# Kernel optimization log

Hardware: AMD Instinct MI355X
Metric: run time of the kernel (lower is better)

The kernel has to match this reference:

```python
import jax, jax.numpy as jnp
import numpy as np

ALPHA = 0.1
EPS = 1e-12  # torch nf.normalize eps


def l2norm(x):
    # F.normalize(x, p=2, dim=-1)
    return x / jnp.maximum(jnp.linalg.norm(x, axis=-1, keepdims=True), EPS)


def setup_inputs() -> dict:
    key = jax.random.key(0)
    ks = jax.random.split(key, 8)
    N, E, F, H1, H2, C = 50000, 600000, 128, 256, 128, 40
    return {
        "x": jax.random.normal(ks[0], (N, F), jnp.float32),
        "neighbor_x": jax.random.normal(ks[1], (E, F), jnp.float32),
        "W1": jax.random.normal(ks[2], (F, H1), jnp.float32) / np.sqrt(F).astype(np.float32),
        "b1": jnp.zeros((H1,), jnp.float32),
        "W2": jax.random.normal(ks[3], (H1, H2), jnp.float32) / np.sqrt(H1).astype(np.float32),
        "b2": jnp.zeros((H2,), jnp.float32),
        "Wc": jax.random.normal(ks[4], (H2, C), jnp.float32) / np.sqrt(H2).astype(np.float32),
        "bc": jnp.zeros((C,), jnp.float32),
        "segment_ids": jax.random.randint(ks[5], (600000,), 0, 50000, dtype=jnp.int32),
    }


def reference(x, neighbor_x, W1, b1, W2, b2, Wc, bc, segment_ids):
    n_nodes = x.shape[0]
    seg_sum = lambda e: jax.ops.segment_sum(e, segment_ids, num_segments=n_nodes)

    # normalize node + neighbor features
    x = l2norm(x)                      # [N, F]
    nb = l2norm(neighbor_x)            # [E, F]

    # tran1 on nodes and neighbors
    h = x @ W1 + b1                    # [N, H1]
    n_h = nb @ W1 + b1                 # [E, H1]

    # app1: x <- (1-a) * (h + sum_neighbors(n_h)) + a * h
    x1 = (1.0 - ALPHA) * (h + seg_sum(n_h)) + ALPHA * h
    # acvt (ReLU; dropout p=0 -> identity) on x and neighbor embeddings
    x1 = jax.nn.relu(x1)
    n_r = jax.nn.relu(n_h)
    # app2: x <- (1-a) * (x + sum_neighbors(relu(n_h))) + a * h
    x2 = (1.0 - ALPHA) * (x1 + seg_sum(n_r)) + ALPHA * h

    # tran2 on nodes and (original tran1'd) neighbors
    h2 = x2 @ W2 + b2                  # [N, H2]
    n_h2 = n_h @ W2 + b2               # [E, H2]

    # app1 again
    x3 = (1.0 - ALPHA) * (h2 + seg_sum(n_h2)) + ALPHA * h2
    x3 = jax.nn.relu(x3)
    n_r2 = jax.nn.relu(n_h2)
    # app2 again
    x4 = (1.0 - ALPHA) * (x3 + seg_sum(n_r2)) + ALPHA * h2

    return x4 @ Wc + bc                # [N, C]
```

## Files before the change

kernel.cpp:

```cpp
#include <hip/hip_runtime.h>

constexpr int F  = 128;
constexpr int H1 = 256;
constexpr int H2 = 128;
constexpr int C  = 40;

using f32x4 = __attribute__((ext_vector_type(4))) float;
using f16x8 = __attribute__((ext_vector_type(8))) _Float16;
using f16x2 = __attribute__((ext_vector_type(2))) _Float16;

__device__ __forceinline__ float wave_sum64(float v) {
#pragma unroll
    for (int off = 32; off > 0; off >>= 1) v += __shfl_xor(v, off, 64);
    return v;
}

__global__ __launch_bounds__(256) void prep_weights(
    const float* __restrict__ W1, const float* __restrict__ W2,
    const float* __restrict__ Wc,
    _Float16* __restrict__ W1t, _Float16* __restrict__ W2t,
    _Float16* __restrict__ Wct)
{
    const int i = blockIdx.x * 256 + threadIdx.x;
    if (i < H1 * F) {
        const int j = i >> 7, f = i & 127;
        W1t[i] = (_Float16)W1[(size_t)f * H1 + j];
    }
    if (i < H2 * H1) {
        const int j = i >> 8, k = i & 255;
        W2t[i] = (_Float16)W2[(size_t)k * H2 + j];
    }
    if (i < 48 * F) {
        const int c = i >> 7, k = i & 127;
        Wct[i] = (c < C) ? (_Float16)Wc[(size_t)k * C + c] : (_Float16)0.f;
    }
}

__global__ __launch_bounds__(256) void k_hist(
    const int* __restrict__ seg, int* __restrict__ hist, int E)
{
    const int e = blockIdx.x * 256 + threadIdx.x;
    if (e < E) atomicAdd(&hist[seg[e]], 1);
}

__global__ __launch_bounds__(256) void k_scan1(
    const int* __restrict__ hist, int* __restrict__ bsum, int N)
{
    __shared__ int s[256];
    const int t = threadIdx.x;
    const int i = blockIdx.x * 256 + t;
    s[t] = (i < N) ? hist[i] : 0;
    __syncthreads();
#pragma unroll
    for (int off = 128; off > 0; off >>= 1) {
        if (t < off) s[t] += s[t + off];
        __syncthreads();
    }
    if (t == 0) bsum[blockIdx.x] = s[0];
}

__global__ __launch_bounds__(256) void k_scan2(int* __restrict__ bsum, int B)
{
    __shared__ int s[256];
    const int t = threadIdx.x;
    const int v = (t < B) ? bsum[t] : 0;
    s[t] = v;
    __syncthreads();
#pragma unroll
    for (int off = 1; off < 256; off <<= 1) {
        const int u = (t >= off) ? s[t - off] : 0;
        __syncthreads();
        s[t] += u;
        __syncthreads();
    }
    if (t < B) bsum[t] = s[t] - v;
}

__global__ __launch_bounds__(256) void k_scan3(
    const int* __restrict__ hist, const int* __restrict__ bsum,
    int* __restrict__ start, int* __restrict__ cursor, int N, int E)
{
    __shared__ int s[256];
    const int t = threadIdx.x;
    const int i = blockIdx.x * 256 + t;
    const int v = (i < N) ? hist[i] : 0;
    s[t] = v;
    __syncthreads();
#pragma unroll
    for (int off = 1; off < 256; off <<= 1) {
        const int u = (t >= off) ? s[t - off] : 0;
        __syncthreads();
        s[t] += u;
        __syncthreads();
    }
    if (i < N) {
        start[i]  = bsum[blockIdx.x] + s[t] - v;
        cursor[i] = 0;
    }
    if (i == 0) start[N] = E;
}

__global__ __launch_bounds__(256) void k_scatter(
    const int* __restrict__ seg, const int* __restrict__ start,
    int* __restrict__ cursor, int* __restrict__ ord, int E)
{
    const int e = blockIdx.x * 256 + threadIdx.x;
    if (e < E) {
        const int s = seg[e];
        const int r = atomicAdd(&cursor[s], 1);
        ord[start[s] + r] = e;
    }
}

__global__ __launch_bounds__(256, 3) void edge_kernel8(
    const float* __restrict__ nbx, const int* __restrict__ seg,
    const int* __restrict__ ord, const int* __restrict__ start,
    const _Float16* __restrict__ W1t, const float* __restrict__ b1,
    const _Float16* __restrict__ W2t, const float* __restrict__ b2,
    float* __restrict__ Sx, float* __restrict__ S2, float* __restrict__ S4,
    int E)
{
    __shared__ _Float16 s_h[64][264];

    const int tid   = threadIdx.x;
    const int lane  = tid & 63;
    const int w     = tid >> 6;
    const int wrow0 = w * 16;
    const int wbase = blockIdx.x * 64 + wrow0;
    const int mrow  = lane & 15;
    const int kgrp  = lane >> 4;

    const int  p    = wbase + mrow;
    const bool pin  = (p < E);
    const int  edge = pin ? ord[p] : 0;

    float va[16][2];
#pragma unroll
    for (int r = 0; r < 16; ++r) {
        const int er = __shfl(edge, r);
        const bool v = (wbase + r < E);
        va[r][0] = v ? nbx[(size_t)er * F + lane] : 0.f;
        va[r][1] = v ? nbx[(size_t)er * F + 64 + lane] : 0.f;
    }

    const int sv = pin ? seg[edge] : -1;
    int fl = 0;
    if (pin) {
        const int s0 = start[sv], s1 = start[sv + 1];
        fl = (s0 >= wbase) && (s1 <= wbase + 16);
    }

#pragma unroll
    for (int r = 0; r < 16; ++r) {
        const float ss = wave_sum64(va[r][0] * va[r][0] + va[r][1] * va[r][1]);
        const float sc = 1.0f / fmaxf(sqrtf(ss), 1e-12f);
        va[r][0] *= sc; va[r][1] *= sc;
        s_h[wrow0 + r][lane]      = (_Float16)va[r][0];
        s_h[wrow0 + r][64 + lane] = (_Float16)va[r][1];
    }

    {
        float a0 = 0.f, a1v = 0.f;
        int cur = __shfl(sv, 0);
        int cf  = __shfl(fl, 0);
#pragma unroll
        for (int r = 0; r < 16; ++r) {
            a0 += va[r][0]; a1v += va[r][1];
            const int nxt = (r < 15) ? __shfl(sv, r + 1) : -2;
            if (nxt != cur) {
                if (cur >= 0) {
                    float* d = &Sx[(size_t)cur * F + lane];
                    if (cf) { d[0] = a0; d[64] = a1v; }
                    else    { atomicAdd(d, a0); atomicAdd(d + 64, a1v); }
                }
                a0 = 0.f; a1v = 0.f; cur = nxt;
                if (r < 15) cf = __shfl(fl, r + 1);
            }
        }
    }

    __syncthreads();

    f16x8 aA[4][4];
#pragma unroll
    for (int m = 0; m < 4; ++m)
#pragma unroll
        for (int kk = 0; kk < 4; ++kk)
            aA[m][kk] = *(const f16x8*)&s_h[m * 16 + mrow][kk * 32 + kgrp * 8];

    asm volatile("s_waitcnt lgkmcnt(0)" ::: "memory");
    __builtin_amdgcn_sched_barrier(0);
    __syncthreads();

    {
        const int colbase = w * 64 + mrow;
        float bj1[4];
#pragma unroll
        for (int ct = 0; ct < 4; ++ct) bj1[ct] = b1[colbase + ct * 16];

        f16x8 b[4], bn[4];
#pragma unroll
        for (int kk = 0; kk < 4; ++kk)
            b[kk] = *(const f16x8*)&W1t[(size_t)colbase * F + kk * 32 + kgrp * 8];

#pragma unroll
        for (int ct = 0; ct < 4; ++ct) {
            const int col = colbase + ct * 16;
            if (ct < 3) {
#pragma unroll
                for (int kk = 0; kk < 4; ++kk)
                    bn[kk] = *(const f16x8*)&W1t[(size_t)(col + 16) * F + kk * 32 + kgrp * 8];
            }
            f32x4 acc[4];
#pragma unroll
            for (int m = 0; m < 4; ++m) acc[m] = (f32x4){0.f, 0.f, 0.f, 0.f};
#pragma unroll
            for (int kk = 0; kk < 4; ++kk)
#pragma unroll
                for (int m = 0; m < 4; ++m)
                    acc[m] = __builtin_amdgcn_mfma_f32_16x16x32_f16(aA[m][kk], b[kk], acc[m], 0, 0, 0);
#pragma unroll
            for (int m = 0; m < 4; ++m)
#pragma unroll
                for (int q = 0; q < 4; ++q)
                    s_h[m * 16 + kgrp * 4 + q][col] = (_Float16)(acc[m][q] + bj1[ct]);
#pragma unroll
            for (int kk = 0; kk < 4; ++kk) b[kk] = bn[kk];
        }
    }
    __syncthreads();

#pragma unroll
    for (int half = 0; half < 2; ++half) {
        const int c0 = half * 128 + 2 * lane;
        float a0 = 0.f, a1v = 0.f;
        int cur = __shfl(sv, 0);
        int cf  = __shfl(fl, 0);
#pragma unroll
        for (int r = 0; r < 16; ++r) {
            const f16x2 pv = *(const f16x2*)&s_h[wrow0 + r][c0];
            a0  += fmaxf((float)pv[0], 0.f);
            a1v += fmaxf((float)pv[1], 0.f);
            const int nxt = (r < 15) ? __shfl(sv, r + 1) : -2;
            if (nxt != cur) {
                if (cur >= 0) {
                    float* d = &S2[(size_t)cur * H1 + c0];
                    if (cf) { *(float2*)d = make_float2(a0, a1v); }
                    else    { atomicAdd(d, a0); atomicAdd(d + 1, a1v); }
                }
                a0 = 0.f; a1v = 0.f; cur = nxt;
                if (r < 15) cf = __shfl(fl, r + 1);
            }
        }
    }

    f32x4 acc2[2][4];
#pragma unroll
    for (int ct = 0; ct < 2; ++ct)
#pragma unroll
        for (int m = 0; m < 4; ++m) acc2[ct][m] = (f32x4){0.f, 0.f, 0.f, 0.f};

    float bj2[2];
#pragma unroll
    for (int ct = 0; ct < 2; ++ct) bj2[ct] = b2[w * 32 + ct * 16 + mrow];

#pragma unroll
    for (int ct = 0; ct < 2; ++ct) {
        const int col = w * 32 + ct * 16 + mrow;
        f16x8 b[8];
#pragma unroll
        for (int k0 = 0; k0 < 8; ++k0)
            b[k0] = *(const f16x8*)&W2t[(size_t)col * H1 + k0 * 32 + kgrp * 8];
#pragma unroll
        for (int m = 0; m < 4; ++m) {
            f16x8 a[8];
#pragma unroll
            for (int k0 = 0; k0 < 8; ++k0)
                a[k0] = *(const f16x8*)&s_h[m * 16 + mrow][k0 * 32 + kgrp * 8];
#pragma unroll
            for (int k0 = 0; k0 < 8; ++k0)
                acc2[ct][m] = __builtin_amdgcn_mfma_f32_16x16x32_f16(a[k0], b[k0], acc2[ct][m], 0, 0, 0);
        }
    }
    __syncthreads();

#pragma unroll
    for (int ct = 0; ct < 2; ++ct) {
        const int col = w * 32 + ct * 16 + mrow;
#pragma unroll
        for (int m = 0; m < 4; ++m)
#pragma unroll
            for (int q = 0; q < 4; ++q)
                s_h[m * 16 + kgrp * 4 + q][col] = (_Float16)(acc2[ct][m][q] + bj2[ct]);
    }
    __syncthreads();

    {
        const int c0 = 2 * lane;
        float a0 = 0.f, a1v = 0.f;
        int cur = __shfl(sv, 0);
        int cf  = __shfl(fl, 0);
#pragma unroll
        for (int r = 0; r < 16; ++r) {
            const f16x2 pv = *(const f16x2*)&s_h[wrow0 + r][c0];
            a0  += fmaxf((float)pv[0], 0.f);
            a1v += fmaxf((float)pv[1], 0.f);
            const int nxt = (r < 15) ? __shfl(sv, r + 1) : -2;
            if (nxt != cur) {
                if (cur >= 0) {
                    float* d = &S4[(size_t)cur * H2 + c0];
                    if (cf) { *(float2*)d = make_float2(a0, a1v); }
                    else    { atomicAdd(d, a0); atomicAdd(d + 1, a1v); }
                }
                a0 = 0.f; a1v = 0.f; cur = nxt;
                if (r < 15) cf = __shfl(fl, r + 1);
            }
        }
    }
}

__global__ __launch_bounds__(256, 2) void node_kernel7(
    const float* __restrict__ x,
    const _Float16* __restrict__ W1t, const float* __restrict__ b1,
    const _Float16* __restrict__ W2t, const float* __restrict__ b2,
    const _Float16* __restrict__ Wct, const float* __restrict__ bc,
    const float* __restrict__ Sx, const float* __restrict__ S2,
    const float* __restrict__ S4, const int* __restrict__ start,
    float* __restrict__ out, int N)
{
    __shared__ _Float16 s_a[4][32][264];

    const int tid  = threadIdx.x;
    const int lane = tid & 63;
    const int w    = tid >> 6;
    const int n0   = blockIdx.x * 64 + w * 16;
    const int mrow = lane & 15;
    const int kgrp = lane >> 4;

#pragma unroll
    for (int r = 0; r < 16; ++r) {
        const int n = n0 + r;
        float v0 = 0.f, v1 = 0.f, u0 = 0.f, u1 = 0.f;
        if (n < N) {
            v0 = x[(size_t)n * F + lane];
            v1 = x[(size_t)n * F + 64 + lane];
            u0 = Sx[(size_t)n * F + lane];
            u1 = Sx[(size_t)n * F + 64 + lane];
        }
        const float ss = wave_sum64(v0 * v0 + v1 * v1);
        const float sc = 1.0f / fmaxf(sqrtf(ss), 1e-12f);
        s_a[w][r][lane]           = (_Float16)(v0 * sc);
        s_a[w][r][64 + lane]      = (_Float16)(v1 * sc);
        s_a[w][16 + r][lane]      = (_Float16)u0;
        s_a[w][16 + r][64 + lane] = (_Float16)u1;
    }

    float cntq[4];
#pragma unroll
    for (int q = 0; q < 4; ++q) {
        const int n = n0 + kgrp * 4 + q;
        cntq[q] = (n < N) ? (float)(start[n + 1] - start[n]) : 0.f;
    }

    asm volatile("s_waitcnt lgkmcnt(0)" ::: "memory");
    __builtin_amdgcn_sched_barrier(0);

    f16x8 aA[2][4];
#pragma unroll
    for (int m = 0; m < 2; ++m)
#pragma unroll
        for (int kk = 0; kk < 4; ++kk)
            aA[m][kk] = *(const f16x8*)&s_a[w][m * 16 + mrow][kk * 32 + kgrp * 8];

#pragma unroll
    for (int n = 0; n < 16; ++n) {
        const int col = n * 16 + mrow;
        f32x4 accH = {0.f, 0.f, 0.f, 0.f};
        f32x4 accS = {0.f, 0.f, 0.f, 0.f};
#pragma unroll
        for (int kk = 0; kk < 4; ++kk) {
            const f16x8 b = *(const f16x8*)&W1t[(size_t)col * F + kk * 32 + kgrp * 8];
            accH = __builtin_amdgcn_mfma_f32_16x16x32_f16(aA[0][kk], b, accH, 0, 0, 0);
            accS = __builtin_amdgcn_mfma_f32_16x16x32_f16(aA[1][kk], b, accS, 0, 0, 0);
        }
        const float bj = b1[col];
#pragma unroll
        for (int q = 0; q < 4; ++q) {
            const int row = kgrp * 4 + q;
            const int n_  = n0 + row;
            const float h  = accH[q] + bj;
            const float S1 = accS[q] + cntq[q] * bj;
            const float x1 = fmaxf(h + 0.9f * S1, 0.f);
            const float s2v = (n_ < N) ? S2[(size_t)n_ * H1 + col] : 0.f;
            const float x2 = 0.9f * (x1 + s2v) + 0.1f * h;
            s_a[w][row][col]      = (_Float16)x2;
            s_a[w][16 + row][col] = (_Float16)S1;
        }
    }

    asm volatile("s_waitcnt lgkmcnt(0)" ::: "memory");
    __builtin_amdgcn_sched_barrier(0);

    f16x8 aB[2][8];
#pragma unroll
    for (int m = 0; m < 2; ++m)
#pragma unroll
        for (int k0 = 0; k0 < 8; ++k0)
            aB[m][k0] = *(const f16x8*)&s_a[w][m * 16 + mrow][k0 * 32 + kgrp * 8];

#pragma unroll
    for (int n = 0; n < 8; ++n) {
        const int col = n * 16 + mrow;
        f32x4 accH = {0.f, 0.f, 0.f, 0.f};
        f32x4 accS = {0.f, 0.f, 0.f, 0.f};
#pragma unroll
        for (int k0 = 0; k0 < 8; ++k0) {
            const f16x8 b = *(const f16x8*)&W2t[(size_t)col * H1 + k0 * 32 + kgrp * 8];
            accH = __builtin_amdgcn_mfma_f32_16x16x32_f16(aB[0][k0], b, accH, 0, 0, 0);
            accS = __builtin_amdgcn_mfma_f32_16x16x32_f16(aB[1][k0], b, accS, 0, 0, 0);
        }
        const float bj = b2[col];
#pragma unroll
        for (int q = 0; q < 4; ++q) {
            const int row = kgrp * 4 + q;
            const int n_  = n0 + row;
            const float h2 = accH[q] + bj;
            const float S3 = accS[q] + cntq[q] * bj;
            const float x3 = fmaxf(h2 + 0.9f * S3, 0.f);
            const float s4v = (n_ < N) ? S4[(size_t)n_ * H2 + col] : 0.f;
            s_a[w][row][col] = (_Float16)(0.9f * (x3 + s4v) + 0.1f * h2);
        }
    }

    asm volatile("s_waitcnt lgkmcnt(0)" ::: "memory");
    __builtin_amdgcn_sched_barrier(0);

    f16x8 aC[4];
#pragma unroll
    for (int kk = 0; kk < 4; ++kk)
        aC[kk] = *(const f16x8*)&s_a[w][mrow][kk * 32 + kgrp * 8];

#pragma unroll
    for (int n = 0; n < 3; ++n) {
        const int col = n * 16 + mrow;
        f32x4 acc = {0.f, 0.f, 0.f, 0.f};
#pragma unroll
        for (int kk = 0; kk < 4; ++kk) {
            const f16x8 b = *(const f16x8*)&Wct[(size_t)col * F + kk * 32 + kgrp * 8];
            acc = __builtin_amdgcn_mfma_f32_16x16x32_f16(aC[kk], b, acc, 0, 0, 0);
        }
        if (col < C) {
            const float bcc = bc[col];
#pragma unroll
            for (int q = 0; q < 4; ++q) {
                const int n_ = n0 + kgrp * 4 + q;
                if (n_ < N) out[(size_t)n_ * C + col] = acc[q] + bcc;
            }
        }
    }
}

extern "C" void kernel_launch(void* const* d_in, const int* in_sizes, int n_in,
                              void* d_out, int out_size, void* d_ws, size_t ws_size,
                              hipStream_t stream) {
    const float* x   = (const float*)d_in[0];
    const float* nbx = (const float*)d_in[1];
    const float* W1  = (const float*)d_in[2];
    const float* b1  = (const float*)d_in[3];
    const float* W2  = (const float*)d_in[4];
    const float* b2  = (const float*)d_in[5];
    const float* Wc  = (const float*)d_in[6];
    const float* bc  = (const float*)d_in[7];
    const int*   seg = (const int*)d_in[8];

    const int N = in_sizes[0] / F;
    const int E = in_sizes[8];
    float* out = (float*)d_out;

    float* Sx    = (float*)d_ws;
    float* S2    = Sx + (size_t)N * F;
    float* S4    = S2 + (size_t)N * H1;
    int*   hist  = (int*)(S4 + (size_t)N * H2);
    int*   cursor= hist + N;
    int*   bsum  = cursor + N;
    int*   start = bsum + 256;
    int*   ord   = start + (N + 1);
    char*  wrest = (char*)(ord + E);
    _Float16* W1t = (_Float16*)(((uintptr_t)wrest + 15) & ~(uintptr_t)15);
    _Float16* W2t = W1t + (size_t)H1 * F;
    _Float16* Wct = W2t + (size_t)H2 * H1;

    const size_t zero_bytes = ((size_t)N * (F + H1 + H2)) * 4 + (size_t)N * 8 + 1024;
    hipMemsetAsync(d_ws, 0, zero_bytes, stream);

    prep_weights<<<128, 256, 0, stream>>>(W1, W2, Wc, W1t, W2t, Wct);

    const int B = (N + 255) / 256;
    k_hist   <<<(E + 255) / 256, 256, 0, stream>>>(seg, hist, E);
    k_scan1  <<<B, 256, 0, stream>>>(hist, bsum, N);
    k_scan2  <<<1, 256, 0, stream>>>(bsum, B);
    k_scan3  <<<B, 256, 0, stream>>>(hist, bsum, start, cursor, N, E);
    k_scatter<<<(E + 255) / 256, 256, 0, stream>>>(seg, start, cursor, ord, E);

    edge_kernel8<<<(E + 63) / 64, 256, 0, stream>>>(
        nbx, seg, ord, start, W1t, b1, W2t, b2, Sx, S2, S4, E);
    node_kernel7<<<(N + 63) / 64, 256, 0, stream>>>(
        x, W1t, b1, W2t, b2, Wct, bc, Sx, S2, S4, start, out, N);
}
```

Before: 565.7 us.

## Process two 64-edge tiles per block with upfront gathers and split LDS buffers

The edge kernel now handles 128 edges per block as two 64-edge tiles. All neighbor-row gathers for both tiles are issued at the start, so the second tile's global loads overlap the first tile's normalization, matmuls and scatter. The single shared buffer becomes two (normalized inputs and layer-1 output), MFMA sections are wrapped in raised wave priority, and A fragments are now read from LDS inside the loop rather than held in registers. This doubles the register footprint for gathered rows, which may hurt occupancy under the 3-block launch bound, and adds more block barriers.

```diff
diff --git a/kernel.cpp b/kernel.cpp
--- a/kernel.cpp
+++ b/kernel.cpp
@@ -112,7 +112,7 @@
     }
 }
 
-__global__ __launch_bounds__(256, 3) void edge_kernel8(
+__global__ __launch_bounds__(256, 3) void edge_kernel9(
     const float* __restrict__ nbx, const int* __restrict__ seg,
     const int* __restrict__ ord, const int* __restrict__ start,
     const _Float16* __restrict__ W1t, const float* __restrict__ b1,
@@ -120,202 +120,196 @@
     float* __restrict__ Sx, float* __restrict__ S2, float* __restrict__ S4,
     int E)
 {
-    __shared__ _Float16 s_h[64][264];
+    __shared__ _Float16 s_nb[64][136];
+    __shared__ _Float16 s_nh[64][264];
 
     const int tid   = threadIdx.x;
     const int lane  = tid & 63;
     const int w     = tid >> 6;
     const int wrow0 = w * 16;
-    const int wbase = blockIdx.x * 64 + wrow0;
     const int mrow  = lane & 15;
     const int kgrp  = lane >> 4;
-
-    const int  p    = wbase + mrow;
-    const bool pin  = (p < E);
-    const int  edge = pin ? ord[p] : 0;
-
-    float va[16][2];
-#pragma unroll
-    for (int r = 0; r < 16; ++r) {
-        const int er = __shfl(edge, r);
-        const bool v = (wbase + r < E);
-        va[r][0] = v ? nbx[(size_t)er * F + lane] : 0.f;
-        va[r][1] = v ? nbx[(size_t)er * F + 64 + lane] : 0.f;
-    }
-
-    const int sv = pin ? seg[edge] : -1;
-    int fl = 0;
-    if (pin) {
-        const int s0 = start[sv], s1 = start[sv + 1];
-        fl = (s0 >= wbase) && (s1 <= wbase + 16);
-    }
-
-#pragma unroll
-    for (int r = 0; r < 16; ++r) {
-        const float ss = wave_sum64(va[r][0] * va[r][0] + va[r][1] * va[r][1]);
-        const float sc = 1.0f / fmaxf(sqrtf(ss), 1e-12f);
-        va[r][0] *= sc; va[r][1] *= sc;
-        s_h[wrow0 + r][lane]      = (_Float16)va[r][0];
-        s_h[wrow0 + r][64 + lane] = (_Float16)va[r][1];
-    }
-
-    {
-        float a0 = 0.f, a1v = 0.f;
-        int cur = __shfl(sv, 0);
-        int cf  = __shfl(fl, 0);
+    const int base  = blockIdx.x * 128;
+
+    int edg[2], sv[2], fl[2];
+    float va[2][16][2];
+#pragma unroll
+    for (int t = 0; t < 2; ++t) {
+        const int wbase = base + t * 64 + wrow0;
+        const int p     = wbase + mrow;
+        const bool pin  = (p < E);
+        edg[t] = pin ? ord[p] : 0;
+        sv[t]  = pin ? seg[edg[t]] : -1;
+        fl[t]  = 0;
+        if (pin) {
+            const int s0 = start[sv[t]], s1 = start[sv[t] + 1];
+            fl[t] = (s0 >= wbase) && (s1 <= wbase + 16);
+        }
 #pragma unroll
         for (int r = 0; r < 16; ++r) {
-            a0 += va[r][0]; a1v += va[r][1];
-            const int nxt = (r < 15) ? __shfl(sv, r + 1) : -2;
-            if (nxt != cur) {
-                if (cur >= 0) {
-                    float* d = &Sx[(size_t)cur * F + lane];
-                    if (cf) { d[0] = a0; d[64] = a1v; }
-                    else    { atomicAdd(d, a0); atomicAdd(d + 64, a1v); }
+            const int er = __shfl(edg[t], r);
+            const bool v = (wbase + r < E);
+            va[t][r][0] = v ? nbx[(size_t)er * F + lane] : 0.f;
+            va[t][r][1] = v ? nbx[(size_t)er * F + 64 + lane] : 0.f;
+        }
+    }
+
+#pragma unroll
+    for (int t = 0; t < 2; ++t) {
+#pragma unroll
+        for (int r = 0; r < 16; ++r) {
+            const float ss = wave_sum64(va[t][r][0] * va[t][r][0] +
+                                        va[t][r][1] * va[t][r][1]);
+            const float sc = 1.0f / fmaxf(sqrtf(ss), 1e-12f);
+            va[t][r][0] *= sc; va[t][r][1] *= sc;
+            s_nb[wrow0 + r][lane]      = (_Float16)va[t][r][0];
+            s_nb[wrow0 + r][64 + lane] = (_Float16)va[t][r][1];
+        }
+
+        {
+            float a0 = 0.f, a1v = 0.f;
+            int cur = __shfl(sv[t], 0);
+            int cf  = __shfl(fl[t], 0);
+#pragma unroll
+            for (int r = 0; r < 16; ++r) {
+                a0 += va[t][r][0]; a1v += va[t][r][1];
+                const int nxt = (r < 15) ? __shfl(sv[t], r + 1) : -2;
+                if (nxt != cur) {
+                    if (cur >= 0) {
+                        float* d = &Sx[(size_t)cur * F + lane];
+                        if (cf) { d[0] = a0; d[64] = a1v; }
+                        else    { atomicAdd(d, a0); atomicAdd(d + 64, a1v); }
+                    }
+                    a0 = 0.f; a1v = 0.f; cur = nxt;
+                    if (r < 15) cf = __shfl(fl[t], r + 1);
                 }
-                a0 = 0.f; a1v = 0.f; cur = nxt;
-                if (r < 15) cf = __shfl(fl, r + 1);
             }
         }
-    }
-
-    __syncthreads();
-
-    f16x8 aA[4][4];
-#pragma unroll
-    for (int m = 0; m < 4; ++m)
-#pragma unroll
-        for (int kk = 0; kk < 4; ++kk)
-            aA[m][kk] = *(const f16x8*)&s_h[m * 16 + mrow][kk * 32 + kgrp * 8];
-
-    asm volatile("s_waitcnt lgkmcnt(0)" ::: "memory");
-    __builtin_amdgcn_sched_barrier(0);
-    __syncthreads();
-
-    {
-        const int colbase = w * 64 + mrow;
-        float bj1[4];
-#pragma unroll
-        for (int ct = 0; ct < 4; ++ct) bj1[ct] = b1[colbase + ct * 16];
-
-        f16x8 b[4], bn[4];
-#pragma unroll
-        for (int kk = 0; kk < 4; ++kk)
-            b[kk] = *(const f16x8*)&W1t[(size_t)colbase * F + kk * 32 + kgrp * 8];
-
-#pragma unroll
-        for (int ct = 0; ct < 4; ++ct) {
-            const int col = colbase + ct * 16;
-            if (ct < 3) {
-#pragma unroll
-                for (int kk = 0; kk < 4; ++kk)
-                    bn[kk] = *(const f16x8*)&W1t[(size_t)(col + 16) * F + kk * 32 + kgrp * 8];
+        __syncthreads();
+
+        {
+            const int colbase = w * 64 + mrow;
+            float bj1[4];
+#pragma unroll
+            for (int ct = 0; ct < 4; ++ct) bj1[ct] = b1[colbase + ct * 16];
+
+            f16x8 b[4], bn[4];
+#pragma unroll
+            for (int kk = 0; kk < 4; ++kk)
+                b[kk] = *(const f16x8*)&W1t[(size_t)colbase * F + kk * 32 + kgrp * 8];
+
+#pragma unroll
+            for (int ct = 0; ct < 4; ++ct) {
+                const int col = colbase + ct * 16;
+                if (ct < 3) {
+#pragma unroll
+                    for (int kk = 0; kk < 4; ++kk)
+                        bn[kk] = *(const f16x8*)&W1t[(size_t)(col + 16) * F + kk * 32 + kgrp * 8];
+                }
+                f32x4 acc[4];
+#pragma unroll
+                for (int m = 0; m < 4; ++m) acc[m] = (f32x4){0.f, 0.f, 0.f, 0.f};
+                __builtin_amdgcn_s_setprio(1);
+#pragma unroll
+                for (int m = 0; m < 4; ++m) {
+                    f16x8 a[4];
+#pragma unroll
+                    for (int kk = 0; kk < 4; ++kk)
+                        a[kk] = *(const f16x8*)&s_nb[m * 16 + mrow][kk * 32 + kgrp * 8];
+#pragma unroll
+                    for (int kk = 0; kk < 4; ++kk)
+                        acc[m] = __builtin_amdgcn_mfma_f32_16x16x32_f16(a[kk], b[kk], acc[m], 0, 0, 0);
+                }
+                __builtin_amdgcn_s_setprio(0);
+#pragma unroll
+                for (int m = 0; m < 4; ++m)
+#pragma unroll
+                    for (int q = 0; q < 4; ++q)
+                        s_nh[m * 16 + kgrp * 4 + q][col] = (_Float16)(acc[m][q] + bj1[ct]);
+#pragma unroll
+                for (int kk = 0; kk < 4; ++kk) b[kk] = bn[kk];
             }
+        }
+        __syncthreads();
+
+#pragma unroll
+        for (int half = 0; half < 2; ++half) {
+            const int c0 = half * 128 + 2 * lane;
+            float a0 = 0.f, a1v = 0.f;
+            int cur = __shfl(sv[t], 0);
+            int cf  = __shfl(fl[t], 0);
+#pragma unroll
+            for (int r = 0; r < 16; ++r) {
+                const f16x2 pv = *(const f16x2*)&s_nh[wrow0 + r][c0];
+                a0  += fmaxf((float)pv[0], 0.f);
+                a1v += fmaxf((float)pv[1], 0.f);
+                const int nxt = (r < 15) ? __shfl(sv[t], r + 1) : -2;
+                if (nxt != cur) {
+                    if (cur >= 0) {
+                        float* d = &S2[(size_t)cur * H1 + c0];
+                        if (cf) { *(float2*)d = make_float2(a0, a1v); }
+                        else    { atomicAdd(d, a0); atomicAdd(d + 1, a1v); }
+                    }
+                    a0 = 0.f; a1v = 0.f; cur = nxt;
+                    if (r < 15) cf = __shfl(fl[t], r + 1);
+                }
+            }
+        }
+
+#pragma unroll
+        for (int ct = 0; ct < 2; ++ct) {
+            const int col = w * 32 + ct * 16 + mrow;
+            const float bj = b2[col];
+            f16x8 b[8];
+#pragma unroll
+            for (int k0 = 0; k0 < 8; ++k0)
+                b[k0] = *(const f16x8*)&W2t[(size_t)col * H1 + k0 * 32 + kgrp * 8];
             f32x4 acc[4];
 #pragma unroll
             for (int m = 0; m < 4; ++m) acc[m] = (f32x4){0.f, 0.f, 0.f, 0.f};
-#pragma unroll
-            for (int kk = 0; kk < 4; ++kk)
-#pragma unroll
-                for (int m = 0; m < 4; ++m)
-                    acc[m] = __builtin_amdgcn_mfma_f32_16x16x32_f16(aA[m][kk], b[kk], acc[m], 0, 0, 0);
+            __builtin_amdgcn_s_setprio(1);
+#pragma unroll
+            for (int m = 0; m < 4; ++m) {
+                f16x8 a[8];
+#pragma unroll
+                for (int k0 = 0; k0 < 8; ++k0)
+                    a[k0] = *(const f16x8*)&s_nh[m * 16 + mrow][k0 * 32 + kgrp * 8];
+#pragma unroll
+                for (int k0 = 0; k0 < 8; ++k0)
+                    acc[m] = __builtin_amdgcn_mfma_f32_16x16x32_f16(a[k0], b[k0], acc[m], 0, 0, 0);
+            }
+            __builtin_amdgcn_s_setprio(0);
 #pragma unroll
             for (int m = 0; m < 4; ++m)
 #pragma unroll
                 for (int q = 0; q < 4; ++q)
-                    s_h[m * 16 + kgrp * 4 + q][col] = (_Float16)(acc[m][q] + bj1[ct]);
-#pragma unroll
-            for (int kk = 0; kk < 4; ++kk) b[kk] = bn[kk];
-        }
-    }
-    __syncthreads();
-
-#pragma unroll
-    for (int half = 0; half < 2; ++half) {
-        const int c0 = half * 128 + 2 * lane;
-        float a0 = 0.f, a1v = 0.f;
-        int cur = __shfl(sv, 0);
-        int cf  = __shfl(fl, 0);
-#pragma unroll
-        for (int r = 0; r < 16; ++r) {
-            const f16x2 pv = *(const f16x2*)&s_h[wrow0 + r][c0];
-            a0  += fmaxf((float)pv[0], 0.f);
-            a1v += fmaxf((float)pv[1], 0.f);
-            const int nxt = (r < 15) ? __shfl(sv, r + 1) : -2;
-            if (nxt != cur) {
-                if (cur >= 0) {
-                    float* d = &S2[(size_t)cur * H1 + c0];
-                    if (cf) { *(float2*)d = make_float2(a0, a1v); }
-                    else    { atomicAdd(d, a0); atomicAdd(d + 1, a1v); }
+                    s_nb[m * 16 + kgrp * 4 + q][col] = (_Float16)(acc[m][q] + bj);
+        }
+        __syncthreads();
+
+        {
+            const int c0 = 2 * lane;
+            float a0 = 0.f, a1v = 0.f;
+            int cur = __shfl(sv[t], 0);
+            int cf  = __shfl(fl[t], 0);
+#pragma unroll
+            for (int r = 0; r < 16; ++r) {
+                const f16x2 pv = *(const f16x2*)&s_nb[wrow0 + r][c0];
+                a0  += fmaxf((float)pv[0], 0.f);
+                a1v += fmaxf((float)pv[1], 0.f);
+                const int nxt = (r < 15) ? __shfl(sv[t], r + 1) : -2;
+                if (nxt != cur) {
+                    if (cur >= 0) {
+                        float* d = &S4[(size_t)cur * H2 + c0];
+                        if (cf) { *(float2*)d = make_float2(a0, a1v); }
+                        else    { atomicAdd(d, a0); atomicAdd(d + 1, a1v); }
+                    }
+                    a0 = 0.f; a1v = 0.f; cur = nxt;
+                    if (r < 15) cf = __shfl(fl[t], r + 1);
                 }
-                a0 = 0.f; a1v = 0.f; cur = nxt;
-                if (r < 15) cf = __shfl(fl, r + 1);
             }
         }
-    }
-
-    f32x4 acc2[2][4];
-#pragma unroll
-    for (int ct = 0; ct < 2; ++ct)
-#pragma unroll
-        for (int m = 0; m < 4; ++m) acc2[ct][m] = (f32x4){0.f, 0.f, 0.f, 0.f};
-
-    float bj2[2];
-#pragma unroll
-    for (int ct = 0; ct < 2; ++ct) bj2[ct] = b2[w * 32 + ct * 16 + mrow];
-
-#pragma unroll
-    for (int ct = 0; ct < 2; ++ct) {
-        const int col = w * 32 + ct * 16 + mrow;
-        f16x8 b[8];
-#pragma unroll
-        for (int k0 = 0; k0 < 8; ++k0)
-            b[k0] = *(const f16x8*)&W2t[(size_t)col * H1 + k0 * 32 + kgrp * 8];
-#pragma unroll
-        for (int m = 0; m < 4; ++m) {
-            f16x8 a[8];
-#pragma unroll
-            for (int k0 = 0; k0 < 8; ++k0)
-                a[k0] = *(const f16x8*)&s_h[m * 16 + mrow][k0 * 32 + kgrp * 8];
-#pragma unroll
-            for (int k0 = 0; k0 < 8; ++k0)
-                acc2[ct][m] = __builtin_amdgcn_mfma_f32_16x16x32_f16(a[k0], b[k0], acc2[ct][m], 0, 0, 0);
-        }
-    }
-    __syncthreads();
-
-#pragma unroll
-    for (int ct = 0; ct < 2; ++ct) {
-        const int col = w * 32 + ct * 16 + mrow;
-#pragma unroll
-        for (int m = 0; m < 4; ++m)
-#pragma unroll
-            for (int q = 0; q < 4; ++q)
-                s_h[m * 16 + kgrp * 4 + q][col] = (_Float16)(acc2[ct][m][q] + bj2[ct]);
-    }
-    __syncthreads();
-
-    {
-        const int c0 = 2 * lane;
-        float a0 = 0.f, a1v = 0.f;
-        int cur = __shfl(sv, 0);
-        int cf  = __shfl(fl, 0);
-#pragma unroll
-        for (int r = 0; r < 16; ++r) {
-            const f16x2 pv = *(const f16x2*)&s_h[wrow0 + r][c0];
-            a0  += fmaxf((float)pv[0], 0.f);
-            a1v += fmaxf((float)pv[1], 0.f);
-            const int nxt = (r < 15) ? __shfl(sv, r + 1) : -2;
-            if (nxt != cur) {
-                if (cur >= 0) {
-                    float* d = &S4[(size_t)cur * H2 + c0];
-                    if (cf) { *(float2*)d = make_float2(a0, a1v); }
-                    else    { atomicAdd(d, a0); atomicAdd(d + 1, a1v); }
-                }
-                a0 = 0.f; a1v = 0.f; cur = nxt;
-                if (r < 15) cf = __shfl(fl, r + 1);
-            }
-        }
+        __syncthreads();
     }
 }
 
@@ -502,7 +496,7 @@
     k_scan3  <<<B, 256, 0, stream>>>(hist, bsum, start, cursor, N, E);
     k_scatter<<<(E + 255) / 256, 256, 0, stream>>>(seg, start, cursor, ord, E);
 
-    edge_kernel8<<<(E + 63) / 64, 256, 0, stream>>>(
+    edge_kernel9<<<(E + 127) / 128, 256, 0, stream>>>(
         nbx, seg, ord, start, W1t, b1, W2t, b2, Sx, S2, S4, E);
     node_kernel7<<<(N + 63) / 64, 256, 0, stream>>>(
         x, W1t, b1, W2t, b2, Wct, bc, Sx, S2, S4, start, out, N);
```

New measurement: 519.9 us. -8.1%, faster.

## Process two edge tiles per block with upfront gathers and raise MFMA priority

Applied to the files above, without the earlier changes.

The edge kernel now handles 128 edges per block as two 64-edge tiles. The indices, segment flags and neighbour rows for both tiles are all gathered before any compute, so the second tile's global loads are in flight while the first tile runs its normalise, GEMM and segment-sum work. The per-tile body is factored into an inlined helper that reuses the same shared buffer, and s_setprio is raised around the MFMA loops so matrix work is favoured over other waves. The cost is higher register pressure from holding a second 32-float tile per lane, which could cause spills or lower occupancy, and half as many blocks are launched.

```diff
diff --git a/kernel.cpp b/kernel.cpp
--- a/kernel.cpp
+++ b/kernel.cpp
@@ -112,43 +112,15 @@
     }
 }
 
-__global__ __launch_bounds__(256, 3) void edge_kernel8(
-    const float* __restrict__ nbx, const int* __restrict__ seg,
-    const int* __restrict__ ord, const int* __restrict__ start,
+__device__ __forceinline__ void process_tile(
+    _Float16 (*s_h)[264],
+    float (&va)[16][2], int sv, int fl,
+    int lane, int w, int mrow, int kgrp,
     const _Float16* __restrict__ W1t, const float* __restrict__ b1,
     const _Float16* __restrict__ W2t, const float* __restrict__ b2,
-    float* __restrict__ Sx, float* __restrict__ S2, float* __restrict__ S4,
-    int E)
-{
-    __shared__ _Float16 s_h[64][264];
-
-    const int tid   = threadIdx.x;
-    const int lane  = tid & 63;
-    const int w     = tid >> 6;
+    float* __restrict__ Sx, float* __restrict__ S2, float* __restrict__ S4)
+{
     const int wrow0 = w * 16;
-    const int wbase = blockIdx.x * 64 + wrow0;
-    const int mrow  = lane & 15;
-    const int kgrp  = lane >> 4;
-
-    const int  p    = wbase + mrow;
-    const bool pin  = (p < E);
-    const int  edge = pin ? ord[p] : 0;
-
-    float va[16][2];
-#pragma unroll
-    for (int r = 0; r < 16; ++r) {
-        const int er = __shfl(edge, r);
-        const bool v = (wbase + r < E);
-        va[r][0] = v ? nbx[(size_t)er * F + lane] : 0.f;
-        va[r][1] = v ? nbx[(size_t)er * F + 64 + lane] : 0.f;
-    }
-
-    const int sv = pin ? seg[edge] : -1;
-    int fl = 0;
-    if (pin) {
-        const int s0 = start[sv], s1 = start[sv + 1];
-        fl = (s0 >= wbase) && (s1 <= wbase + 16);
-    }
 
 #pragma unroll
     for (int r = 0; r < 16; ++r) {
@@ -178,7 +150,6 @@
             }
         }
     }
-
     __syncthreads();
 
     f16x8 aA[4][4];
@@ -214,11 +185,13 @@
             f32x4 acc[4];
 #pragma unroll
             for (int m = 0; m < 4; ++m) acc[m] = (f32x4){0.f, 0.f, 0.f, 0.f};
+            __builtin_amdgcn_s_setprio(1);
 #pragma unroll
             for (int kk = 0; kk < 4; ++kk)
 #pragma unroll
                 for (int m = 0; m < 4; ++m)
                     acc[m] = __builtin_amdgcn_mfma_f32_16x16x32_f16(aA[m][kk], b[kk], acc[m], 0, 0, 0);
+            __builtin_amdgcn_s_setprio(0);
 #pragma unroll
             for (int m = 0; m < 4; ++m)
 #pragma unroll
@@ -271,6 +244,7 @@
 #pragma unroll
         for (int k0 = 0; k0 < 8; ++k0)
             b[k0] = *(const f16x8*)&W2t[(size_t)col * H1 + k0 * 32 + kgrp * 8];
+        __builtin_amdgcn_s_setprio(1);
 #pragma unroll
         for (int m = 0; m < 4; ++m) {
             f16x8 a[8];
@@ -281,6 +255,7 @@
             for (int k0 = 0; k0 < 8; ++k0)
                 acc2[ct][m] = __builtin_amdgcn_mfma_f32_16x16x32_f16(a[k0], b[k0], acc2[ct][m], 0, 0, 0);
         }
+        __builtin_amdgcn_s_setprio(0);
     }
     __syncthreads();
 
@@ -319,6 +294,61 @@
     }
 }
 
+__global__ __launch_bounds__(256, 3) void edge_kernel10(
+    const float* __restrict__ nbx, const int* __restrict__ seg,
+    const int* __restrict__ ord, const int* __restrict__ start,
+    const _Float16* __restrict__ W1t, const float* __restrict__ b1,
+    const _Float16* __restrict__ W2t, const float* __restrict__ b2,
+    float* __restrict__ Sx, float* __restrict__ S2, float* __restrict__ S4,
+    int E)
+{
+    __shared__ _Float16 s_h[64][264];
+
+    const int tid   = threadIdx.x;
+    const int lane  = tid & 63;
+    const int w     = tid >> 6;
+    const int wrow0 = w * 16;
+    const int mrow  = lane & 15;
+    const int kgrp  = lane >> 4;
+    const int base  = blockIdx.x * 128;
+
+    int edg[2], sv[2], fl[2];
+#pragma unroll
+    for (int t = 0; t < 2; ++t) {
+        const int wbase = base + t * 64 + wrow0;
+        const int p     = wbase + mrow;
+        const bool pin  = (p < E);
+        edg[t] = pin ? ord[p] : 0;
+        sv[t]  = pin ? seg[edg[t]] : -1;
+        fl[t]  = 0;
+        if (pin) {
+            const int s0 = start[sv[t]], s1 = start[sv[t] + 1];
+            fl[t] = (s0 >= wbase) && (s1 <= wbase + 16);
+        }
+    }
+
+    float va0[16][2], va1[16][2];
+#pragma unroll
+    for (int r = 0; r < 16; ++r) {
+        const int er = __shfl(edg[0], r);
+        const bool v = (base + wrow0 + r < E);
+        va0[r][0] = v ? nbx[(size_t)er * F + lane] : 0.f;
+        va0[r][1] = v ? nbx[(size_t)er * F + 64 + lane] : 0.f;
+    }
+#pragma unroll
+    for (int r = 0; r < 16; ++r) {
+        const int er = __shfl(edg[1], r);
+        const bool v = (base + 64 + wrow0 + r < E);
+        va1[r][0] = v ? nbx[(size_t)er * F + lane] : 0.f;
+        va1[r][1] = v ? nbx[(size_t)er * F + 64 + lane] : 0.f;
+    }
+
+    process_tile(s_h, va0, sv[0], fl[0], lane, w, mrow, kgrp,
+                 W1t, b1, W2t, b2, Sx, S2, S4);
+    process_tile(s_h, va1, sv[1], fl[1], lane, w, mrow, kgrp,
+                 W1t, b1, W2t, b2, Sx, S2, S4);
+}
+
 __global__ __launch_bounds__(256, 2) void node_kernel7(
     const float* __restrict__ x,
     const _Float16* __restrict__ W1t, const float* __restrict__ b1,
@@ -502,7 +532,7 @@
     k_scan3  <<<B, 256, 0, stream>>>(hist, bsum, start, cursor, N, E);
     k_scatter<<<(E + 255) / 256, 256, 0, stream>>>(seg, start, cursor, ord, E);
 
-    edge_kernel8<<<(E + 63) / 64, 256, 0, stream>>>(
+    edge_kernel10<<<(E + 127) / 128, 256, 0, stream>>>(
         nbx, seg, ord, start, W1t, b1, W2t, b2, Sx, S2, S4, E);
     node_kernel7<<<(N + 63) / 64, 256, 0, stream>>>(
         x, W1t, b1, W2t, b2, Wct, bc, Sx, S2, S4, start, out, N);
```

Result: slower. 597.1 us (+5.5%).
